# Kernel tuning notes

Hardware: AMD Instinct MI355X
Metric: run time of the kernel (lower is better)

## Reference

```python
import jax, jax.numpy as jnp
import numpy as np

B, T, C = 2, 2048, 2048
N_HEADS, HEAD_DIM, N_KV_HEADS = 16, 128, 4
N_REP = N_HEADS // N_KV_HEADS
WINDOW = 512
EPS = 1e-6
THETA = 10000.0


def setup_inputs() -> dict:
    key = jax.random.key(0)
    ks = jax.random.split(key, 6)
    x = jax.random.normal(ks[0], (B, T, C), dtype=jnp.float32)
    norm_w = jnp.ones((C,), dtype=jnp.float32)
    wq = jax.random.normal(ks[1], (C, N_HEADS * HEAD_DIM), dtype=jnp.float32) * 0.02
    wk = jax.random.normal(ks[2], (C, N_KV_HEADS * HEAD_DIM), dtype=jnp.float32) * 0.02
    wv = jax.random.normal(ks[3], (C, N_KV_HEADS * HEAD_DIM), dtype=jnp.float32) * 0.02
    wo = jax.random.normal(ks[4], (N_HEADS * HEAD_DIM, C), dtype=jnp.float32) * 0.02
    # precompute_rope: freqs over half head_dim, outer with positions
    inv = 1.0 / (THETA ** (np.arange(0, HEAD_DIM, 2, dtype=np.float32) / HEAD_DIM))
    t = np.arange(T, dtype=np.float32)
    freqs = np.outer(t, inv)  # (T, HEAD_DIM/2)
    rope_cos = jnp.asarray(np.cos(freqs), dtype=jnp.float32)
    rope_sin = jnp.asarray(np.sin(freqs), dtype=jnp.float32)
    return {"x": x, "norm_w": norm_w, "wq": wq, "wk": wk, "wv": wv, "wo": wo,
            "rope_cos": rope_cos, "rope_sin": rope_sin}


def _rmsnorm(x, w):
    xf = x.astype(jnp.float32)
    norm = jax.lax.rsqrt(jnp.mean(xf * xf, axis=-1, keepdims=True) + EPS)
    return (xf * norm).astype(x.dtype) * w


def _rotate(x, cos, sin):
    # x: (B,H,T,D); cos/sin: (1,1,T,D/2). Half-split RoPE as in apply_rope.
    d = x.shape[-1] // 2
    x1, x2 = x[..., :d], x[..., d:]
    return jnp.concatenate([x1 * cos - x2 * sin, x2 * cos + x1 * sin], axis=-1)


def reference(x, norm_w, wq, wk, wv, wo, rope_cos, rope_sin):
    normed = _rmsnorm(x, norm_w)
    q = (normed @ wq).reshape(B, T, N_HEADS, HEAD_DIM).transpose(0, 2, 1, 3)
    k = (normed @ wk).reshape(B, T, N_KV_HEADS, HEAD_DIM).transpose(0, 2, 1, 3)
    v = (normed @ wv).reshape(B, T, N_KV_HEADS, HEAD_DIM).transpose(0, 2, 1, 3)
    cos = rope_cos[None, None, :T, :]
    sin = rope_sin[None, None, :T, :]
    q = _rotate(q, cos, sin)
    k = _rotate(k, cos, sin)
    # GQA: repeat each kv head contiguously (matches expand+reshape)
    k = jnp.repeat(k, N_REP, axis=1)
    v = jnp.repeat(v, N_REP, axis=1)
    scale = 1.0 / jnp.sqrt(jnp.float32(HEAD_DIM))
    scores = jnp.einsum('bhtd,bhsd->bhts', q, k) * scale  # (B,H,T,T)
    # causal + sliding window mask (S == T, offset == 0)
    row = jnp.arange(T)[:, None]
    col = jnp.arange(T)[None, :]
    mask = (col <= row) & (row - col < WINDOW)  # (T,T) bool
    scores = jnp.where(mask[None, None, :, :], scores, -jnp.inf)
    attn = jax.nn.softmax(scores, axis=-1)
    out = jnp.einsum('bhts,bhsd->bhtd', attn, v)
    out = out.transpose(0, 2, 1, 3).reshape(B, T, N_HEADS * HEAD_DIM)
    return x + out @ wo
```

## Files before the change

### kernel.cpp

```cpp
#include <hip/hip_runtime.h>
#include <hip/hip_bf16.h>

typedef __attribute__((ext_vector_type(8))) __bf16 bf16x8;
typedef __attribute__((ext_vector_type(4))) __bf16 bf16x4;
typedef __attribute__((ext_vector_type(4))) float f32x4;

#define BDIM 2
#define TSEQ 2048
#define CDIM 2048
#define NH 16
#define NKV 4
#define HD 128
#define WIN 512

__device__ __forceinline__ void gl_lds16(const __bf16* g, __bf16* l) {
  __builtin_amdgcn_global_load_lds(
      (const __attribute__((address_space(1))) void*)g,
      (__attribute__((address_space(3))) void*)l, 16, 0, 0);
}

__global__ __launch_bounds__(256) void k_rmsnorm(const float* __restrict__ x,
                                                 const float* __restrict__ w,
                                                 __bf16* __restrict__ xn) {
  __shared__ float red[4];
  const int row = blockIdx.x;
  const int tid = threadIdx.x;
  const float* xr = x + (size_t)row * CDIM;
  f32x4 v0 = *reinterpret_cast<const f32x4*>(&xr[tid * 8]);
  f32x4 v1 = *reinterpret_cast<const f32x4*>(&xr[tid * 8 + 4]);
  float s = v0[0] * v0[0] + v0[1] * v0[1] + v0[2] * v0[2] + v0[3] * v0[3] +
            v1[0] * v1[0] + v1[1] * v1[1] + v1[2] * v1[2] + v1[3] * v1[3];
#pragma unroll
  for (int off = 32; off > 0; off >>= 1) s += __shfl_down(s, off, 64);
  if ((tid & 63) == 0) red[tid >> 6] = s;
  __syncthreads();
  float tot = red[0] + red[1] + red[2] + red[3];
  float nrm = rsqrtf(tot * (1.0f / CDIM) + 1e-6f);
  const float* wp = w + tid * 8;
  bf16x8 o;
  o[0] = (__bf16)(v0[0] * nrm * wp[0]);
  o[1] = (__bf16)(v0[1] * nrm * wp[1]);
  o[2] = (__bf16)(v0[2] * nrm * wp[2]);
  o[3] = (__bf16)(v0[3] * nrm * wp[3]);
  o[4] = (__bf16)(v1[0] * nrm * wp[4]);
  o[5] = (__bf16)(v1[1] * nrm * wp[5]);
  o[6] = (__bf16)(v1[2] * nrm * wp[6]);
  o[7] = (__bf16)(v1[3] * nrm * wp[7]);
  *reinterpret_cast<bf16x8*>(&xn[(size_t)row * CDIM + tid * 8]) = o;
}

__global__ __launch_bounds__(256) void k_wtrans_all(
    const float* __restrict__ wq, const float* __restrict__ wk,
    const float* __restrict__ wv, const float* __restrict__ wo,
    __bf16* __restrict__ wqT, __bf16* __restrict__ wkT,
    __bf16* __restrict__ wvT, __bf16* __restrict__ woT) {
  __shared__ float lt[64][65];
  const int bx = blockIdx.x;
  const float* W;
  __bf16* Wt;
  int N, ntile;
  if (bx < 32) { W = wq; Wt = wqT; N = 2048; ntile = bx; }
  else if (bx < 40) { W = wk; Wt = wkT; N = 512; ntile = bx - 32; }
  else if (bx < 48) { W = wv; Wt = wvT; N = 512; ntile = bx - 40; }
  else { W = wo; Wt = woT; N = 2048; ntile = bx - 48; }
  const int tid = threadIdx.x;
  const int n0 = ntile * 64, k0 = blockIdx.y * 64;
  const int tr = tid >> 4, tc = tid & 15;
#pragma unroll
  for (int i = 0; i < 4; ++i) {
    int kr = tr + i * 16;
    f32x4 vv = *reinterpret_cast<const f32x4*>(&W[(size_t)(k0 + kr) * N + n0 + tc * 4]);
    lt[kr][tc * 4 + 0] = vv[0];
    lt[kr][tc * 4 + 1] = vv[1];
    lt[kr][tc * 4 + 2] = vv[2];
    lt[kr][tc * 4 + 3] = vv[3];
  }
  __syncthreads();
#pragma unroll
  for (int i = 0; i < 4; ++i) {
    int nr = tr + i * 16;
    int kc = tc * 4;
    bf16x4 o;
    o[0] = (__bf16)lt[kc + 0][nr];
    o[1] = (__bf16)lt[kc + 1][nr];
    o[2] = (__bf16)lt[kc + 2][nr];
    o[3] = (__bf16)lt[kc + 3][nr];
    *reinterpret_cast<bf16x4*>(&Wt[(size_t)(n0 + nr) * 2048 + k0 + kc]) = o;
  }
}

__global__ __launch_bounds__(256) void k_rope(__bf16* __restrict__ Q,
                                              __bf16* __restrict__ K,
                                              const float* __restrict__ rc,
                                              const float* __restrict__ rs) {
  int g = blockIdx.x * 4 + (threadIdx.x >> 6);
  int lane = threadIdx.x & 63;
  int b = g / (TSEQ * (NH + NKV));
  int rem = g % (TSEQ * (NH + NKV));
  int t = rem / (NH + NKV);
  int hh = rem % (NH + NKV);
  __bf16* base;
  if (hh < NH)
    base = Q + (((size_t)(b * NH + hh)) * TSEQ + t) * HD;
  else
    base = K + (((size_t)(b * NKV + (hh - NH))) * TSEQ + t) * HD;
  float x1 = (float)base[lane];
  float x2 = (float)base[lane + 64];
  float c = rc[t * 64 + lane];
  float s = rs[t * 64 + lane];
  base[lane] = (__bf16)(x1 * c - x2 * s);
  base[lane + 64] = (__bf16)(x2 * c + x1 * s);
}

__global__ __launch_bounds__(256) void k_gemm_qkv(
    const __bf16* __restrict__ xn, const __bf16* __restrict__ wqT,
    const __bf16* __restrict__ wkT, const __bf16* __restrict__ wvT,
    __bf16* __restrict__ Q, __bf16* __restrict__ K, __bf16* __restrict__ VT) {
  __shared__ __align__(16) __bf16 lmem[128 * 136];
  __bf16* lA = lmem;
  __bf16* lB = lmem + 128 * 32;
  const int tid = threadIdx.x;
  const int lane = tid & 63;
  const int w = tid >> 6;
  const int wrow = (w >> 1) * 64, wcol = (w & 1) * 64;
  const int l16 = lane & 15, lhi = lane >> 4;
  const int grow = lane >> 2;
  const int gcol = (lane & 3) * 8;
  const int m0 = blockIdx.y * 128;
  const int n0 = blockIdx.x * 128;
  const __bf16* wt;
  int nrel;
  if (n0 < 2048) { wt = wqT; nrel = n0; }
  else if (n0 < 2560) { wt = wkT; nrel = n0 - 2048; }
  else { wt = wvT; nrel = n0 - 2560; }

  f32x4 acc[4][4] = {};

  for (int k0 = 0; k0 < CDIM; k0 += 32) {
#pragma unroll
    for (int i = 0; i < 2; ++i) {
      const int r0 = (w * 2 + i) * 16;
      gl_lds16(&xn[(size_t)(m0 + r0 + grow) * CDIM + k0 + gcol], &lA[r0 * 32]);
      gl_lds16(&wt[(size_t)(nrel + r0 + grow) * CDIM + k0 + gcol], &lB[r0 * 32]);
    }
    __syncthreads();
    bf16x8 a[4], b[4];
#pragma unroll
    for (int mi = 0; mi < 4; ++mi)
      a[mi] = *reinterpret_cast<const bf16x8*>(&lA[(wrow + mi * 16 + l16) * 32 + lhi * 8]);
#pragma unroll
    for (int ni = 0; ni < 4; ++ni)
      b[ni] = *reinterpret_cast<const bf16x8*>(&lB[(wcol + ni * 16 + l16) * 32 + lhi * 8]);
#pragma unroll
    for (int mi = 0; mi < 4; ++mi)
#pragma unroll
      for (int ni = 0; ni < 4; ++ni)
        acc[mi][ni] = __builtin_amdgcn_mfma_f32_16x16x32_bf16(a[mi], b[ni], acc[mi][ni], 0, 0, 0);
    __syncthreads();
  }

  const int bb = m0 >> 11;
  if (n0 < 2560) {
#pragma unroll
    for (int mi = 0; mi < 4; ++mi) {
#pragma unroll
      for (int ni = 0; ni < 4; ++ni) {
#pragma unroll
        for (int r = 0; r < 4; ++r) {
          int row = m0 + wrow + mi * 16 + lhi * 4 + r;
          int col = n0 + wcol + ni * 16 + l16;
          int t = row & 2047;
          __bf16 hv = (__bf16)acc[mi][ni][r];
          if (n0 < 2048) {
            int h = col >> 7, d = col & 127;
            Q[(((size_t)(bb * NH + h)) * TSEQ + t) * HD + d] = hv;
          } else {
            int h = (col - 2048) >> 7, d = col & 127;
            K[(((size_t)(bb * NKV + h)) * TSEQ + t) * HD + d] = hv;
          }
        }
      }
    }
  } else {
#pragma unroll
    for (int mi = 0; mi < 4; ++mi)
#pragma unroll
      for (int ni = 0; ni < 4; ++ni)
#pragma unroll
        for (int r = 0; r < 4; ++r)
          lmem[(size_t)(wcol + ni * 16 + l16) * 136 + wrow + mi * 16 + lhi * 4 + r] =
              (__bf16)acc[mi][ni][r];
    __syncthreads();
    const int h = (n0 - 2560) >> 7;
    const size_t vbase = ((size_t)(bb * NKV + h)) * HD * TSEQ;
    const int t0 = m0 & 2047;
#pragma unroll
    for (int it = 0; it < 8; ++it) {
      int d = it * 16 + (tid >> 4);
      int tt = (tid & 15) * 8;
      bf16x8 vv = *reinterpret_cast<const bf16x8*>(&lmem[(size_t)d * 136 + tt]);
      *reinterpret_cast<bf16x8*>(&VT[vbase + (size_t)d * TSEQ + t0 + tt]) = vv;
    }
  }
}

#define SWZ(row, col) ((col) ^ (((row) & 7) << 3))
#define LPS 72

__global__ __launch_bounds__(256) void k_attn(const __bf16* __restrict__ Q,
                                              const __bf16* __restrict__ K,
                                              const __bf16* __restrict__ VT,
                                              __bf16* __restrict__ Aout) {
  __shared__ __align__(16) __bf16 lK[64 * 128];
  __shared__ __align__(16) __bf16 lVt[128 * 64];
  __shared__ __align__(16) __bf16 lP[4][32][LPS];

  const int tid = threadIdx.x, lane = tid & 63, wid = tid >> 6;
  const int l16 = lane & 15, lhi = lane >> 4;
  const int bh = blockIdx.y;
  const int b = bh >> 4, h = bh & 15;
  const int kvh = h >> 2;
  const int qb = 15 - blockIdx.x;
  const int q0 = qb * 128;
  const int qw = q0 + wid * 32;

  const __bf16* Qb = Q + (size_t)bh * TSEQ * HD;
  const __bf16* Kb = K + (size_t)(b * NKV + kvh) * TSEQ * HD;
  const __bf16* Vt = VT + (size_t)(b * NKV + kvh) * HD * TSEQ;

  bf16x8 aq[2][4];
#pragma unroll
  for (int mi = 0; mi < 2; ++mi)
#pragma unroll
    for (int dblk = 0; dblk < 4; ++dblk)
      aq[mi][dblk] = *reinterpret_cast<const bf16x8*>(
          &Qb[(size_t)(qw + mi * 16 + l16) * HD + dblk * 32 + lhi * 8]);

  float mrow[2] = {-INFINITY, -INFINITY};
  float lrow[2] = {0.0f, 0.0f};
  f32x4 accO[2][8] = {};

  int s_lo = q0 - (WIN - 1);
  if (s_lo < 0) s_lo = 0;
  s_lo &= ~63;
  const int nt = (q0 + 128 - s_lo) >> 6;
  const float scale = 0.08838834764831845f;

  bf16x8 kreg[4], vreg[4];
#pragma unroll
  for (int i = 0; i < 4; ++i) {
    int slot = tid + i * 256;
    kreg[i] = *reinterpret_cast<const bf16x8*>(
        &Kb[(size_t)(s_lo + (slot >> 4)) * HD + (slot & 15) * 8]);
    vreg[i] = *reinterpret_cast<const bf16x8*>(
        &Vt[(size_t)(slot >> 3) * TSEQ + s_lo + (slot & 7) * 8]);
  }

  for (int t = 0; t < nt; ++t) {
    const int s0 = s_lo + t * 64;
    __syncthreads();
#pragma unroll
    for (int i = 0; i < 4; ++i) {
      int slot = tid + i * 256;
      int kr = slot >> 4, kc = (slot & 15) * 8;
      *reinterpret_cast<bf16x8*>(&lK[kr * 128 + SWZ(kr, kc)]) = kreg[i];
      int vd = slot >> 3, vc = (slot & 7) * 8;
      *reinterpret_cast<bf16x8*>(&lVt[vd * 64 + SWZ(vd, vc)]) = vreg[i];
    }
    if (t + 1 < nt) {
      const int s1 = s0 + 64;
#pragma unroll
      for (int i = 0; i < 4; ++i) {
        int slot = tid + i * 256;
        kreg[i] = *reinterpret_cast<const bf16x8*>(
            &Kb[(size_t)(s1 + (slot >> 4)) * HD + (slot & 15) * 8]);
        vreg[i] = *reinterpret_cast<const bf16x8*>(
            &Vt[(size_t)(slot >> 3) * TSEQ + s1 + (slot & 7) * 8]);
      }
    }
    __syncthreads();

    f32x4 accT[2][4] = {};
    __builtin_amdgcn_s_setprio(1);
#pragma unroll
    for (int sb = 0; sb < 4; ++sb) {
#pragma unroll
      for (int dblk = 0; dblk < 4; ++dblk) {
        int srow = sb * 16 + l16, scol = dblk * 32 + lhi * 8;
        bf16x8 bk = *reinterpret_cast<const bf16x8*>(&lK[srow * 128 + SWZ(srow, scol)]);
        accT[0][sb] = __builtin_amdgcn_mfma_f32_16x16x32_bf16(bk, aq[0][dblk], accT[0][sb], 0, 0, 0);
        accT[1][sb] = __builtin_amdgcn_mfma_f32_16x16x32_bf16(bk, aq[1][dblk], accT[1][sb], 0, 0, 0);
      }
    }
    __builtin_amdgcn_s_setprio(0);

#pragma unroll
    for (int mi = 0; mi < 2; ++mi) {
      const int qrow = qw + mi * 16 + l16;
      float pv[4][4];
      float tmax = -INFINITY;
#pragma unroll
      for (int sb = 0; sb < 4; ++sb) {
#pragma unroll
        for (int r = 0; r < 4; ++r) {
          int sc = s0 + sb * 16 + lhi * 4 + r;
          float val = accT[mi][sb][r] * scale;
          bool ok = (sc <= qrow) && (qrow - sc < WIN);
          val = ok ? val : -INFINITY;
          pv[sb][r] = val;
          tmax = fmaxf(tmax, val);
        }
      }
      tmax = fmaxf(tmax, __shfl_xor(tmax, 16, 64));
      tmax = fmaxf(tmax, __shfl_xor(tmax, 32, 64));

      bool defer = __all(tmax <= mrow[mi] + 8.0f);
      float mnew = mrow[mi];
      if (!defer) {
        mnew = fmaxf(mrow[mi], tmax);
        float corr = (mrow[mi] == mnew) ? 1.0f : __expf(mrow[mi] - mnew);
        mrow[mi] = mnew;
        lrow[mi] *= corr;
        float corrR[4];
#pragma unroll
        for (int r = 0; r < 4; ++r) corrR[r] = __shfl(corr, lhi * 4 + r, 64);
#pragma unroll
        for (int ni = 0; ni < 8; ++ni)
#pragma unroll
          for (int r = 0; r < 4; ++r) accO[mi][ni][r] *= corrR[r];
      }
      float msafe = (mnew == -INFINITY) ? 0.0f : mnew;
      float psum = 0.0f;
#pragma unroll
      for (int sb = 0; sb < 4; ++sb) {
        bf16x4 pk;
#pragma unroll
        for (int r = 0; r < 4; ++r) {
          float p = __expf(pv[sb][r] - msafe);
          psum += p;
          pk[r] = (__bf16)p;
        }
        *reinterpret_cast<bf16x4*>(&lP[wid][mi * 16 + l16][sb * 16 + lhi * 4]) = pk;
      }
      psum += __shfl_xor(psum, 16, 64);
      psum += __shfl_xor(psum, 32, 64);
      lrow[mi] += psum;
    }

    bf16x8 ap[2][2];
#pragma unroll
    for (int mi = 0; mi < 2; ++mi)
#pragma unroll
      for (int ks = 0; ks < 2; ++ks)
        ap[mi][ks] = *reinterpret_cast<const bf16x8*>(&lP[wid][mi * 16 + l16][ks * 32 + lhi * 8]);
    __builtin_amdgcn_s_setprio(1);
#pragma unroll
    for (int ni = 0; ni < 8; ++ni) {
      int vrow = ni * 16 + l16;
      bf16x8 bv0 = *reinterpret_cast<const bf16x8*>(&lVt[vrow * 64 + SWZ(vrow, lhi * 8)]);
      bf16x8 bv1 = *reinterpret_cast<const bf16x8*>(&lVt[vrow * 64 + SWZ(vrow, 32 + lhi * 8)]);
      accO[0][ni] = __builtin_amdgcn_mfma_f32_16x16x32_bf16(ap[0][0], bv0, accO[0][ni], 0, 0, 0);
      accO[0][ni] = __builtin_amdgcn_mfma_f32_16x16x32_bf16(ap[0][1], bv1, accO[0][ni], 0, 0, 0);
      accO[1][ni] = __builtin_amdgcn_mfma_f32_16x16x32_bf16(ap[1][0], bv0, accO[1][ni], 0, 0, 0);
      accO[1][ni] = __builtin_amdgcn_mfma_f32_16x16x32_bf16(ap[1][1], bv1, accO[1][ni], 0, 0, 0);
    }
    __builtin_amdgcn_s_setprio(0);
  }

#pragma unroll
  for (int mi = 0; mi < 2; ++mi) {
    float invl = 1.0f / lrow[mi];
    float invlR[4];
#pragma unroll
    for (int r = 0; r < 4; ++r) invlR[r] = __shfl(invl, lhi * 4 + r, 64);
#pragma unroll
    for (int ni = 0; ni < 8; ++ni) {
#pragma unroll
      for (int r = 0; r < 4; ++r) {
        int row = qw + mi * 16 + lhi * 4 + r;
        int d = ni * 16 + l16;
        Aout[((size_t)(b * TSEQ + row)) * CDIM + h * HD + d] = (__bf16)(accO[mi][ni][r] * invlR[r]);
      }
    }
  }
}

__global__ __launch_bounds__(256) void k_gemm_out(const __bf16* __restrict__ A,
                                                  const __bf16* __restrict__ woT,
                                                  const float* __restrict__ x,
                                                  float* __restrict__ out) {
  __shared__ __align__(16) __bf16 lA[128 * 32];
  __shared__ __align__(16) __bf16 lB[128 * 32];
  const int tid = threadIdx.x;
  const int lane = tid & 63;
  const int w = tid >> 6;
  const int wrow = (w >> 1) * 64, wcol = (w & 1) * 64;
  const int l16 = lane & 15, lhi = lane >> 4;
  const int grow = lane >> 2;
  const int gcol = (lane & 3) * 8;
  const int m0 = blockIdx.y * 128;
  const int n0 = blockIdx.x * 128;

  f32x4 acc[4][4] = {};

  for (int k0 = 0; k0 < CDIM; k0 += 32) {
#pragma unroll
    for (int i = 0; i < 2; ++i) {
      const int r0 = (w * 2 + i) * 16;
      gl_lds16(&A[(size_t)(m0 + r0 + grow) * CDIM + k0 + gcol], &lA[r0 * 32]);
      gl_lds16(&woT[(size_t)(n0 + r0 + grow) * CDIM + k0 + gcol], &lB[r0 * 32]);
    }
    __syncthreads();
    bf16x8 a[4], b[4];
#pragma unroll
    for (int mi = 0; mi < 4; ++mi)
      a[mi] = *reinterpret_cast<const bf16x8*>(&lA[(wrow + mi * 16 + l16) * 32 + lhi * 8]);
#pragma unroll
    for (int ni = 0; ni < 4; ++ni)
      b[ni] = *reinterpret_cast<const bf16x8*>(&lB[(wcol + ni * 16 + l16) * 32 + lhi * 8]);
#pragma unroll
    for (int mi = 0; mi < 4; ++mi)
#pragma unroll
      for (int ni = 0; ni < 4; ++ni)
        acc[mi][ni] = __builtin_amdgcn_mfma_f32_16x16x32_bf16(a[mi], b[ni], acc[mi][ni], 0, 0, 0);
    __syncthreads();
  }

#pragma unroll
  for (int mi = 0; mi < 4; ++mi) {
#pragma unroll
    for (int ni = 0; ni < 4; ++ni) {
#pragma unroll
      for (int r = 0; r < 4; ++r) {
        int row = m0 + wrow + mi * 16 + lhi * 4 + r;
        int col = n0 + wcol + ni * 16 + l16;
        size_t idx = (size_t)row * CDIM + col;
        out[idx] = x[idx] + acc[mi][ni][r];
      }
    }
  }
}

extern "C" void kernel_launch(void* const* d_in, const int* in_sizes, int n_in,
                              void* d_out, int out_size, void* d_ws, size_t ws_size,
                              hipStream_t stream) {
  const float* x = (const float*)d_in[0];
  const float* norm_w = (const float*)d_in[1];
  const float* wq = (const float*)d_in[2];
  const float* wk = (const float*)d_in[3];
  const float* wv = (const float*)d_in[4];
  const float* wo = (const float*)d_in[5];
  const float* rc = (const float*)d_in[6];
  const float* rs = (const float*)d_in[7];
  float* out = (float*)d_out;

  char* ws = (char*)d_ws;
  __bf16* xn  = (__bf16*)(ws);
  __bf16* wqT = (__bf16*)(ws + 16777216);
  __bf16* wkT = (__bf16*)(ws + 25165824);
  __bf16* wvT = (__bf16*)(ws + 27262976);
  __bf16* woT = (__bf16*)(ws + 29360128);
  __bf16* Qb  = (__bf16*)(ws + 37748736);
  __bf16* Kb  = (__bf16*)(ws + 54525952);
  __bf16* VTb = (__bf16*)(ws + 58720256);
  if (ws_size < 62914560) return;

  k_wtrans_all<<<dim3(80, 32), 256, 0, stream>>>(wq, wk, wv, wo, wqT, wkT, wvT, woT);
  k_rmsnorm<<<4096, 256, 0, stream>>>(x, norm_w, xn);
  k_gemm_qkv<<<dim3(24, 32), 256, 0, stream>>>(xn, wqT, wkT, wvT, Qb, Kb, VTb);
  k_rope<<<(BDIM * TSEQ * (NH + NKV)) / 4, 256, 0, stream>>>(Qb, Kb, rc, rs);
  k_attn<<<dim3(16, BDIM * NH), 256, 0, stream>>>(Qb, Kb, VTb, xn);
  k_gemm_out<<<dim3(16, 32), 256, 0, stream>>>(xn, woT, x, out);
}
```

Measured before the change: 304.8 us.

## Fuse RoPE into QKV GEMM epilogue and double attention waves per block

The QKV GEMM now tiles each wave as 32 rows by the full 128 columns, so both halves of every head are held by the same lane and RoPE can be applied in the epilogue. This removes the separate k_rope kernel and its extra read and write of Q and K. The attention kernel moves to 512 threads with 16 query rows per wave, halving per-wave accumulator registers and K/V staging per thread, which raises parallelism per block. In exchange, each GEMM wave reloads all of B from LDS, and attention issues more LDS traffic per MFMA.

```diff
diff --git a/kernel.cpp b/kernel.cpp
--- a/kernel.cpp
+++ b/kernel.cpp
@@ -89,32 +89,10 @@
   }
 }
 
-__global__ __launch_bounds__(256) void k_rope(__bf16* __restrict__ Q,
-                                              __bf16* __restrict__ K,
-                                              const float* __restrict__ rc,
-                                              const float* __restrict__ rs) {
-  int g = blockIdx.x * 4 + (threadIdx.x >> 6);
-  int lane = threadIdx.x & 63;
-  int b = g / (TSEQ * (NH + NKV));
-  int rem = g % (TSEQ * (NH + NKV));
-  int t = rem / (NH + NKV);
-  int hh = rem % (NH + NKV);
-  __bf16* base;
-  if (hh < NH)
-    base = Q + (((size_t)(b * NH + hh)) * TSEQ + t) * HD;
-  else
-    base = K + (((size_t)(b * NKV + (hh - NH))) * TSEQ + t) * HD;
-  float x1 = (float)base[lane];
-  float x2 = (float)base[lane + 64];
-  float c = rc[t * 64 + lane];
-  float s = rs[t * 64 + lane];
-  base[lane] = (__bf16)(x1 * c - x2 * s);
-  base[lane + 64] = (__bf16)(x2 * c + x1 * s);
-}
-
 __global__ __launch_bounds__(256) void k_gemm_qkv(
     const __bf16* __restrict__ xn, const __bf16* __restrict__ wqT,
     const __bf16* __restrict__ wkT, const __bf16* __restrict__ wvT,
+    const float* __restrict__ rc, const float* __restrict__ rs,
     __bf16* __restrict__ Q, __bf16* __restrict__ K, __bf16* __restrict__ VT) {
   __shared__ __align__(16) __bf16 lmem[128 * 136];
   __bf16* lA = lmem;
@@ -122,7 +100,7 @@
   const int tid = threadIdx.x;
   const int lane = tid & 63;
   const int w = tid >> 6;
-  const int wrow = (w >> 1) * 64, wcol = (w & 1) * 64;
+  const int wrow = w * 32;
   const int l16 = lane & 15, lhi = lane >> 4;
   const int grow = lane >> 2;
   const int gcol = (lane & 3) * 8;
@@ -134,7 +112,7 @@
   else if (n0 < 2560) { wt = wkT; nrel = n0 - 2048; }
   else { wt = wvT; nrel = n0 - 2560; }
 
-  f32x4 acc[4][4] = {};
+  f32x4 acc[2][8] = {};
 
   for (int k0 = 0; k0 < CDIM; k0 += 32) {
 #pragma unroll
@@ -144,51 +122,55 @@
       gl_lds16(&wt[(size_t)(nrel + r0 + grow) * CDIM + k0 + gcol], &lB[r0 * 32]);
     }
     __syncthreads();
-    bf16x8 a[4], b[4];
-#pragma unroll
-    for (int mi = 0; mi < 4; ++mi)
+    bf16x8 a[2], b[8];
+#pragma unroll
+    for (int mi = 0; mi < 2; ++mi)
       a[mi] = *reinterpret_cast<const bf16x8*>(&lA[(wrow + mi * 16 + l16) * 32 + lhi * 8]);
 #pragma unroll
-    for (int ni = 0; ni < 4; ++ni)
-      b[ni] = *reinterpret_cast<const bf16x8*>(&lB[(wcol + ni * 16 + l16) * 32 + lhi * 8]);
-#pragma unroll
-    for (int mi = 0; mi < 4; ++mi)
-#pragma unroll
-      for (int ni = 0; ni < 4; ++ni)
+    for (int ni = 0; ni < 8; ++ni)
+      b[ni] = *reinterpret_cast<const bf16x8*>(&lB[(ni * 16 + l16) * 32 + lhi * 8]);
+#pragma unroll
+    for (int mi = 0; mi < 2; ++mi)
+#pragma unroll
+      for (int ni = 0; ni < 8; ++ni)
         acc[mi][ni] = __builtin_amdgcn_mfma_f32_16x16x32_bf16(a[mi], b[ni], acc[mi][ni], 0, 0, 0);
     __syncthreads();
   }
 
   const int bb = m0 >> 11;
   if (n0 < 2560) {
-#pragma unroll
-    for (int mi = 0; mi < 4; ++mi) {
-#pragma unroll
-      for (int ni = 0; ni < 4; ++ni) {
-#pragma unroll
-        for (int r = 0; r < 4; ++r) {
-          int row = m0 + wrow + mi * 16 + lhi * 4 + r;
-          int col = n0 + wcol + ni * 16 + l16;
-          int t = row & 2047;
-          __bf16 hv = (__bf16)acc[mi][ni][r];
-          if (n0 < 2048) {
-            int h = col >> 7, d = col & 127;
-            Q[(((size_t)(bb * NH + h)) * TSEQ + t) * HD + d] = hv;
-          } else {
-            int h = (col - 2048) >> 7, d = col & 127;
-            K[(((size_t)(bb * NKV + h)) * TSEQ + t) * HD + d] = hv;
-          }
+    const bool isQ = (n0 < 2048);
+    const int h = isQ ? (n0 >> 7) : ((n0 - 2048) >> 7);
+    __bf16* outb = isQ ? (Q + (((size_t)(bb * NH + h)) * TSEQ) * HD)
+                       : (K + (((size_t)(bb * NKV + h)) * TSEQ) * HD);
+#pragma unroll
+    for (int mi = 0; mi < 2; ++mi) {
+#pragma unroll
+      for (int r = 0; r < 4; ++r) {
+        int row = m0 + wrow + mi * 16 + lhi * 4 + r;
+        int t = row & 2047;
+        __bf16* op = outb + (size_t)t * HD;
+        const float* cp = rc + t * 64;
+        const float* sp = rs + t * 64;
+#pragma unroll
+        for (int ni = 0; ni < 4; ++ni) {
+          int d = ni * 16 + l16;
+          float c = cp[d], s = sp[d];
+          float x1 = acc[mi][ni][r];
+          float x2 = acc[mi][ni + 4][r];
+          op[d] = (__bf16)(x1 * c - x2 * s);
+          op[d + 64] = (__bf16)(x2 * c + x1 * s);
         }
       }
     }
   } else {
 #pragma unroll
-    for (int mi = 0; mi < 4; ++mi)
-#pragma unroll
-      for (int ni = 0; ni < 4; ++ni)
+    for (int mi = 0; mi < 2; ++mi)
+#pragma unroll
+      for (int ni = 0; ni < 8; ++ni)
 #pragma unroll
         for (int r = 0; r < 4; ++r)
-          lmem[(size_t)(wcol + ni * 16 + l16) * 136 + wrow + mi * 16 + lhi * 4 + r] =
+          lmem[(size_t)(ni * 16 + l16) * 136 + wrow + mi * 16 + lhi * 4 + r] =
               (__bf16)acc[mi][ni][r];
     __syncthreads();
     const int h = (n0 - 2560) >> 7;
@@ -207,13 +189,13 @@
 #define SWZ(row, col) ((col) ^ (((row) & 7) << 3))
 #define LPS 72
 
-__global__ __launch_bounds__(256) void k_attn(const __bf16* __restrict__ Q,
-                                              const __bf16* __restrict__ K,
-                                              const __bf16* __restrict__ VT,
-                                              __bf16* __restrict__ Aout) {
+__global__ __launch_bounds__(512, 4) void k_attn(const __bf16* __restrict__ Q,
+                                                 const __bf16* __restrict__ K,
+                                                 const __bf16* __restrict__ VT,
+                                                 __bf16* __restrict__ Aout) {
   __shared__ __align__(16) __bf16 lK[64 * 128];
   __shared__ __align__(16) __bf16 lVt[128 * 64];
-  __shared__ __align__(16) __bf16 lP[4][32][LPS];
+  __shared__ __align__(16) __bf16 lP[8][16][LPS];
 
   const int tid = threadIdx.x, lane = tid & 63, wid = tid >> 6;
   const int l16 = lane & 15, lhi = lane >> 4;
@@ -222,23 +204,21 @@
   const int kvh = h >> 2;
   const int qb = 15 - blockIdx.x;
   const int q0 = qb * 128;
-  const int qw = q0 + wid * 32;
+  const int qw = q0 + wid * 16;
 
   const __bf16* Qb = Q + (size_t)bh * TSEQ * HD;
   const __bf16* Kb = K + (size_t)(b * NKV + kvh) * TSEQ * HD;
   const __bf16* Vt = VT + (size_t)(b * NKV + kvh) * HD * TSEQ;
 
-  bf16x8 aq[2][4];
-#pragma unroll
-  for (int mi = 0; mi < 2; ++mi)
-#pragma unroll
-    for (int dblk = 0; dblk < 4; ++dblk)
-      aq[mi][dblk] = *reinterpret_cast<const bf16x8*>(
-          &Qb[(size_t)(qw + mi * 16 + l16) * HD + dblk * 32 + lhi * 8]);
-
-  float mrow[2] = {-INFINITY, -INFINITY};
-  float lrow[2] = {0.0f, 0.0f};
-  f32x4 accO[2][8] = {};
+  bf16x8 aq[4];
+#pragma unroll
+  for (int dblk = 0; dblk < 4; ++dblk)
+    aq[dblk] = *reinterpret_cast<const bf16x8*>(
+        &Qb[(size_t)(qw + l16) * HD + dblk * 32 + lhi * 8]);
+
+  float mrow = -INFINITY;
+  float lrow = 0.0f;
+  f32x4 accO[8] = {};
 
   int s_lo = q0 - (WIN - 1);
   if (s_lo < 0) s_lo = 0;
@@ -246,10 +226,10 @@
   const int nt = (q0 + 128 - s_lo) >> 6;
   const float scale = 0.08838834764831845f;
 
-  bf16x8 kreg[4], vreg[4];
-#pragma unroll
-  for (int i = 0; i < 4; ++i) {
-    int slot = tid + i * 256;
+  bf16x8 kreg[2], vreg[2];
+#pragma unroll
+  for (int i = 0; i < 2; ++i) {
+    int slot = tid + i * 512;
     kreg[i] = *reinterpret_cast<const bf16x8*>(
         &Kb[(size_t)(s_lo + (slot >> 4)) * HD + (slot & 15) * 8]);
     vreg[i] = *reinterpret_cast<const bf16x8*>(
@@ -260,8 +240,8 @@
     const int s0 = s_lo + t * 64;
     __syncthreads();
 #pragma unroll
-    for (int i = 0; i < 4; ++i) {
-      int slot = tid + i * 256;
+    for (int i = 0; i < 2; ++i) {
+      int slot = tid + i * 512;
       int kr = slot >> 4, kc = (slot & 15) * 8;
       *reinterpret_cast<bf16x8*>(&lK[kr * 128 + SWZ(kr, kc)]) = kreg[i];
       int vd = slot >> 3, vc = (slot & 7) * 8;
@@ -270,8 +250,8 @@
     if (t + 1 < nt) {
       const int s1 = s0 + 64;
 #pragma unroll
-      for (int i = 0; i < 4; ++i) {
-        int slot = tid + i * 256;
+      for (int i = 0; i < 2; ++i) {
+        int slot = tid + i * 512;
         kreg[i] = *reinterpret_cast<const bf16x8*>(
             &Kb[(size_t)(s1 + (slot >> 4)) * HD + (slot & 15) * 8]);
         vreg[i] = *reinterpret_cast<const bf16x8*>(
@@ -280,7 +260,7 @@
     }
     __syncthreads();
 
-    f32x4 accT[2][4] = {};
+    f32x4 accT[4] = {};
     __builtin_amdgcn_s_setprio(1);
 #pragma unroll
     for (int sb = 0; sb < 4; ++sb) {
@@ -288,15 +268,13 @@
       for (int dblk = 0; dblk < 4; ++dblk) {
         int srow = sb * 16 + l16, scol = dblk * 32 + lhi * 8;
         bf16x8 bk = *reinterpret_cast<const bf16x8*>(&lK[srow * 128 + SWZ(srow, scol)]);
-        accT[0][sb] = __builtin_amdgcn_mfma_f32_16x16x32_bf16(bk, aq[0][dblk], accT[0][sb], 0, 0, 0);
-        accT[1][sb] = __builtin_amdgcn_mfma_f32_16x16x32_bf16(bk, aq[1][dblk], accT[1][sb], 0, 0, 0);
+        accT[sb] = __builtin_amdgcn_mfma_f32_16x16x32_bf16(bk, aq[dblk], accT[sb], 0, 0, 0);
       }
     }
     __builtin_amdgcn_s_setprio(0);
 
-#pragma unroll
-    for (int mi = 0; mi < 2; ++mi) {
-      const int qrow = qw + mi * 16 + l16;
+    {
+      const int qrow = qw + l16;
       float pv[4][4];
       float tmax = -INFINITY;
 #pragma unroll
@@ -304,7 +282,7 @@
 #pragma unroll
         for (int r = 0; r < 4; ++r) {
           int sc = s0 + sb * 16 + lhi * 4 + r;
-          float val = accT[mi][sb][r] * scale;
+          float val = accT[sb][r] * scale;
           bool ok = (sc <= qrow) && (qrow - sc < WIN);
           val = ok ? val : -INFINITY;
           pv[sb][r] = val;
@@ -314,20 +292,20 @@
       tmax = fmaxf(tmax, __shfl_xor(tmax, 16, 64));
       tmax = fmaxf(tmax, __shfl_xor(tmax, 32, 64));
 
-      bool defer = __all(tmax <= mrow[mi] + 8.0f);
-      float mnew = mrow[mi];
+      bool defer = __all(tmax <= mrow + 8.0f);
+      float mnew = mrow;
       if (!defer) {
-        mnew = fmaxf(mrow[mi], tmax);
-        float corr = (mrow[mi] == mnew) ? 1.0f : __expf(mrow[mi] - mnew);
-        mrow[mi] = mnew;
-        lrow[mi] *= corr;
+        mnew = fmaxf(mrow, tmax);
+        float corr = (mrow == mnew) ? 1.0f : __expf(mrow - mnew);
+        mrow = mnew;
+        lrow *= corr;
         float corrR[4];
 #pragma unroll
         for (int r = 0; r < 4; ++r) corrR[r] = __shfl(corr, lhi * 4 + r, 64);
 #pragma unroll
         for (int ni = 0; ni < 8; ++ni)
 #pragma unroll
-          for (int r = 0; r < 4; ++r) accO[mi][ni][r] *= corrR[r];
+          for (int r = 0; r < 4; ++r) accO[ni][r] *= corrR[r];
       }
       float msafe = (mnew == -INFINITY) ? 0.0f : mnew;
       float psum = 0.0f;
@@ -340,36 +318,31 @@
           psum += p;
           pk[r] = (__bf16)p;
         }
-        *reinterpret_cast<bf16x4*>(&lP[wid][mi * 16 + l16][sb * 16 + lhi * 4]) = pk;
+        *reinterpret_cast<bf16x4*>(&lP[wid][l16][sb * 16 + lhi * 4]) = pk;
       }
       psum += __shfl_xor(psum, 16, 64);
       psum += __shfl_xor(psum, 32, 64);
-      lrow[mi] += psum;
-    }
-
-    bf16x8 ap[2][2];
-#pragma unroll
-    for (int mi = 0; mi < 2; ++mi)
-#pragma unroll
-      for (int ks = 0; ks < 2; ++ks)
-        ap[mi][ks] = *reinterpret_cast<const bf16x8*>(&lP[wid][mi * 16 + l16][ks * 32 + lhi * 8]);
+      lrow += psum;
+    }
+
+    bf16x8 ap[2];
+#pragma unroll
+    for (int ks = 0; ks < 2; ++ks)
+      ap[ks] = *reinterpret_cast<const bf16x8*>(&lP[wid][l16][ks * 32 + lhi * 8]);
     __builtin_amdgcn_s_setprio(1);
 #pragma unroll
     for (int ni = 0; ni < 8; ++ni) {
       int vrow = ni * 16 + l16;
       bf16x8 bv0 = *reinterpret_cast<const bf16x8*>(&lVt[vrow * 64 + SWZ(vrow, lhi * 8)]);
       bf16x8 bv1 = *reinterpret_cast<const bf16x8*>(&lVt[vrow * 64 + SWZ(vrow, 32 + lhi * 8)]);
-      accO[0][ni] = __builtin_amdgcn_mfma_f32_16x16x32_bf16(ap[0][0], bv0, accO[0][ni], 0, 0, 0);
-      accO[0][ni] = __builtin_amdgcn_mfma_f32_16x16x32_bf16(ap[0][1], bv1, accO[0][ni], 0, 0, 0);
-      accO[1][ni] = __builtin_amdgcn_mfma_f32_16x16x32_bf16(ap[1][0], bv0, accO[1][ni], 0, 0, 0);
-      accO[1][ni] = __builtin_amdgcn_mfma_f32_16x16x32_bf16(ap[1][1], bv1, accO[1][ni], 0, 0, 0);
+      accO[ni] = __builtin_amdgcn_mfma_f32_16x16x32_bf16(ap[0], bv0, accO[ni], 0, 0, 0);
+      accO[ni] = __builtin_amdgcn_mfma_f32_16x16x32_bf16(ap[1], bv1, accO[ni], 0, 0, 0);
     }
     __builtin_amdgcn_s_setprio(0);
   }
 
-#pragma unroll
-  for (int mi = 0; mi < 2; ++mi) {
-    float invl = 1.0f / lrow[mi];
+  {
+    float invl = 1.0f / lrow;
     float invlR[4];
 #pragma unroll
     for (int r = 0; r < 4; ++r) invlR[r] = __shfl(invl, lhi * 4 + r, 64);
@@ -377,9 +350,9 @@
     for (int ni = 0; ni < 8; ++ni) {
 #pragma unroll
       for (int r = 0; r < 4; ++r) {
-        int row = qw + mi * 16 + lhi * 4 + r;
+        int row = qw + lhi * 4 + r;
         int d = ni * 16 + l16;
-        Aout[((size_t)(b * TSEQ + row)) * CDIM + h * HD + d] = (__bf16)(accO[mi][ni][r] * invlR[r]);
+        Aout[((size_t)(b * TSEQ + row)) * CDIM + h * HD + d] = (__bf16)(accO[ni][r] * invlR[r]);
       }
     }
   }
@@ -467,8 +440,7 @@
 
   k_wtrans_all<<<dim3(80, 32), 256, 0, stream>>>(wq, wk, wv, wo, wqT, wkT, wvT, woT);
   k_rmsnorm<<<4096, 256, 0, stream>>>(x, norm_w, xn);
-  k_gemm_qkv<<<dim3(24, 32), 256, 0, stream>>>(xn, wqT, wkT, wvT, Qb, Kb, VTb);
-  k_rope<<<(BDIM * TSEQ * (NH + NKV)) / 4, 256, 0, stream>>>(Qb, Kb, rc, rs);
-  k_attn<<<dim3(16, BDIM * NH), 256, 0, stream>>>(Qb, Kb, VTb, xn);
+  k_gemm_qkv<<<dim3(24, 32), 256, 0, stream>>>(xn, wqT, wkT, wvT, rc, rs, Qb, Kb, VTb);
+  k_attn<<<dim3(16, BDIM * NH), 512, 0, stream>>>(Qb, Kb, VTb, xn);
   k_gemm_out<<<dim3(16, 32), 256, 0, stream>>>(xn, woT, x, out);
 }
```

Measured after the change: 276.6 us. 1.1x faster.
